# Performance work log

Measured on AMD Instinct MI355X. Metric: run time of the kernel, lower is better.

## Reference

```python
import jax, jax.numpy as jnp
import numpy as np

NUM_JOINTS = 140
NUM_VERTICES = 13059
NUM_BONES = 28
BATCH = 512


def euler_zyx_to_rot(e):
    """e: [..., 3] Euler angles in (z, y, x) order -> [..., 3, 3] with R = Rz @ Ry @ Rx."""
    z, y, x = e[..., 0], e[..., 1], e[..., 2]
    cx, sx = jnp.cos(x), jnp.sin(x)
    cy, sy = jnp.cos(y), jnp.sin(y)
    cz, sz = jnp.cos(z), jnp.sin(z)
    r00 = cz * cy
    r01 = cz * sy * sx - sz * cx
    r02 = cz * sy * cx + sz * sx
    r10 = sz * cy
    r11 = sz * sy * sx + cz * cx
    r12 = sz * sy * cx - cz * sx
    r20 = -sy
    r21 = cy * sx
    r22 = cy * cx
    R = jnp.stack([r00, r01, r02, r10, r11, r12, r20, r21, r22], axis=-1)
    return R.reshape(e.shape[:-1] + (3, 3))


def _mouse_forward(pose, bone_lengths, center_bone_length, trans, scale,
                   v_template, t_pose_joints, weights, parent, bone_mapper):
    B = pose.shape[0]
    Jn = NUM_JOINTS
    dt = pose.dtype

    bl = jax.nn.sigmoid(bone_lengths / 5.0) * 2.0            # [B, 28]
    R = euler_zyx_to_rot(pose.reshape(B, Jn, 3))             # [B, J, 3, 3]
    Jt = t_pose_joints                                       # [J, 3]

    # bone offsets for joints 1..J-1, scaled per bone_length_mapper
    off = Jt[1:] - Jt[parent[1:]]                            # [J-1, 3]
    blid = bone_mapper[1:]                                   # [J-1]
    bl_g = jnp.where(blid[None, :] >= 0,
                     jnp.take(bl, jnp.maximum(blid, 0), axis=1),
                     jnp.ones((), dt))                       # [B, J-1]
    # joint index 1 (position 0 in the [J-1] arrays) uses center_bone_length
    scale_per = bl_g.at[:, 0].set(center_bone_length[:, 0])
    off_b = off[None] * scale_per[..., None]                 # [B, J-1, 3]

    bottom = jnp.broadcast_to(jnp.array([0., 0., 0., 1.], dt), (B, Jn - 1, 1, 4))
    top = jnp.concatenate([R[:, 1:], off_b[..., None]], axis=-1)   # [B, J-1, 3, 4]
    A = jnp.concatenate([top, bottom], axis=-2)              # [B, J-1, 4, 4] local transforms

    root_t = jnp.broadcast_to(Jt[0], (B, 3))[..., None]      # [B, 3, 1]
    root_top = jnp.concatenate([R[:, 0], root_t], axis=-1)   # [B, 3, 4]
    root_bot = jnp.broadcast_to(jnp.array([0., 0., 0., 1.], dt), (B, 1, 4))
    G0 = jnp.concatenate([root_top, root_bot], axis=-2)      # [B, 4, 4]

    G_init = jnp.zeros((B, Jn, 4, 4), dt).at[:, 0].set(G0)

    def step(G, xs):
        i, p, Ai = xs                                        # Ai: [B, 4, 4]
        Gp = jnp.take(G, p, axis=1)                          # [B, 4, 4]
        Gi = Gp @ Ai
        return G.at[:, i].set(Gi), None

    idx = jnp.arange(1, Jn)
    G, _ = jax.lax.scan(step, G_init, (idx, parent[1:], jnp.swapaxes(A, 0, 1)))

    J_final = G[:, :, :3, 3]                                 # [B, J, 3]

    # subtract rest-pose joint contribution (relative transforms for LBS)
    Jh = jnp.concatenate([jnp.broadcast_to(Jt, (B, Jn, 3)),
                          jnp.zeros((B, Jn, 1), dt)], axis=-1)      # [B, J, 4]
    d = jnp.einsum('bjmn,bjn->bjm', G, Jh)                   # [B, J, 4]
    G_rel = jnp.concatenate([G[..., :3], (G[..., 3] - d)[..., None]], axis=-1)

    # linear blend skinning
    T = jnp.einsum('vj,bjmn->bvmn', weights, G_rel)          # [B, V, 4, 4]
    vh = jnp.concatenate([v_template, jnp.ones((NUM_VERTICES, 1), dt)], axis=-1)
    V = jnp.einsum('bvmn,vn->bvm', T[:, :, :3, :], vh)       # [B, V, 3]

    s = scale[:, 0][:, None, None]
    V = V * s + trans[:, None, :]
    J_out = J_final * s + trans[:, None, :]
    return V, J_out


def setup_inputs() -> dict:
    key = jax.random.key(0)
    ks = jax.random.split(key, 8)
    rng = np.random.default_rng(0)
    parent = np.zeros(NUM_JOINTS, dtype=np.int32)
    for i in range(1, NUM_JOINTS):
        parent[i] = rng.integers(0, i)                       # valid kinematic tree
    bone_mapper = rng.integers(-1, NUM_BONES, size=NUM_JOINTS).astype(np.int32)
    W = jax.random.uniform(ks[6], (NUM_VERTICES, NUM_JOINTS), jnp.float32)
    W = W / jnp.sum(W, axis=1, keepdims=True)                # row-stochastic skinning weights
    return {
        'pose': jax.random.normal(ks[0], (BATCH, NUM_JOINTS * 3), jnp.float32) * 0.2,
        'bone_lengths': jax.random.normal(ks[1], (BATCH, NUM_BONES), jnp.float32),
        'center_bone_length': jax.random.uniform(ks[2], (BATCH, 1), jnp.float32, 0.5, 1.5),
        'trans': jax.random.normal(ks[3], (BATCH, 3), jnp.float32),
        'scale': jax.random.uniform(ks[4], (BATCH, 1), jnp.float32, 0.5, 1.5),
        'v_template': jax.random.normal(ks[5], (NUM_VERTICES, 3), jnp.float32),
        't_pose_joints': jax.random.normal(ks[7], (NUM_JOINTS, 3), jnp.float32),
        'weights': W,
        'parent': jnp.asarray(parent),
        'bone_mapper': jnp.asarray(bone_mapper),
    }


def reference(pose, bone_lengths, center_bone_length, trans, scale,
              v_template, t_pose_joints, weights, parent, bone_mapper):
    return _mouse_forward(pose, bone_lengths, center_bone_length, trans, scale,
                          v_template, t_pose_joints, weights, parent, bone_mapper)
```

## Files before the change

kernel.cpp:

```cpp
#include <hip/hip_runtime.h>
#include <math.h>

#define NJ 140
#define NV 13059
#define NB 512
#define NBONES 28

#define MTILES 103
#define NBLK 12
#define KS 18
#define GRID_GEMM (MTILES*NBLK)

#define APREP_SLOTS (MTILES*KS*512)

typedef _Float16 f16x8 __attribute__((ext_vector_type(8)));
typedef float    f32x4 __attribute__((ext_vector_type(4)));

#define GL16(gp, lp) __builtin_amdgcn_global_load_lds( \
    (const __attribute__((address_space(1))) unsigned int*)(gp), \
    (__attribute__((address_space(3))) unsigned int*)(lp), 16, 0, 0)

__global__ __launch_bounds__(256) void prep_kernel(
    const float* __restrict__ pose,
    const float* __restrict__ bone_lengths,
    const float* __restrict__ cbl,
    const float* __restrict__ trans,
    const float* __restrict__ scale,
    const float* __restrict__ v_template,
    const float* __restrict__ t_pose,
    const int*   __restrict__ parent,
    const int*   __restrict__ bone_mapper,
    const float* __restrict__ weights,
    _Float16* __restrict__ Ap,
    _Float16* __restrict__ Bp,
    float* __restrict__ jout)
{
    const int t = threadIdx.x;

    if (blockIdx.x >= NB) {
        const int id  = blockIdx.x - NB;
        const int mt  = id / KS;
        const int ks  = id - mt*KS;
        const int row = t >> 1;
        const int q   = t & 1;
        const int v   = mt*128 + row;
        const int j0  = ks*8 + q*4;
        const int s   = (row >> 1) & 3;

        f16x8 oA, oB;
        #pragma unroll
        for (int i = 0; i < 8; ++i) { oA[i] = (_Float16)0.f; oB[i] = (_Float16)0.f; }

        if (v < NV && j0 + 3 < NJ) {
            float x = v_template[v*3+0];
            float y = v_template[v*3+1];
            float z = v_template[v*3+2];
            const float4 w4 = *(const float4*)(weights + (size_t)v*NJ + j0);
            oA[0] = (_Float16)(w4.x*x); oA[1] = (_Float16)(w4.x*y);
            oA[2] = (_Float16)(w4.x*z); oA[3] = (_Float16)w4.x;
            oA[4] = (_Float16)(w4.y*x); oA[5] = (_Float16)(w4.y*y);
            oA[6] = (_Float16)(w4.y*z); oA[7] = (_Float16)w4.y;
            oB[0] = (_Float16)(w4.z*x); oB[1] = (_Float16)(w4.z*y);
            oB[2] = (_Float16)(w4.z*z); oB[3] = (_Float16)w4.z;
            oB[4] = (_Float16)(w4.w*x); oB[5] = (_Float16)(w4.w*y);
            oB[6] = (_Float16)(w4.w*z); oB[7] = (_Float16)w4.w;
        }
        const int base = ((2*q) ^ s) & ~1;
        _Float16* dst = Ap + (((size_t)id)*512 + row*4 + base)*8;
        if (s & 1) {
            *(f16x8*)dst       = oB;
            *(f16x8*)(dst + 8) = oA;
        } else {
            *(f16x8*)dst       = oA;
            *(f16x8*)(dst + 8) = oB;
        }
        return;
    }

    __shared__ float M0[NJ][12];
    __shared__ float M1[NJ][12];
    __shared__ int   a0[NJ];
    __shared__ int   a1[NJ];

    const int b = blockIdx.x;

    if (t < NJ) {
        const int j = t;
        float z = pose[b*(NJ*3) + 3*j + 0];
        float y = pose[b*(NJ*3) + 3*j + 1];
        float x = pose[b*(NJ*3) + 3*j + 2];
        float cx = cosf(x), sx = sinf(x);
        float cy = cosf(y), sy = sinf(y);
        float cz = cosf(z), sz = sinf(z);
        float r00 = cz*cy;
        float r01 = cz*sy*sx - sz*cx;
        float r02 = cz*sy*cx + sz*sx;
        float r10 = sz*cy;
        float r11 = sz*sy*sx + cz*cx;
        float r12 = sz*sy*cx - cz*sx;
        float r20 = -sy;
        float r21 = cy*sx;
        float r22 = cy*cx;
        float t0, t1, t2;
        int p = parent[j];
        if (j == 0) {
            t0 = t_pose[0]; t1 = t_pose[1]; t2 = t_pose[2];
        } else {
            float ox = t_pose[3*j+0] - t_pose[3*p+0];
            float oy = t_pose[3*j+1] - t_pose[3*p+1];
            float oz = t_pose[3*j+2] - t_pose[3*p+2];
            float s;
            if (j == 1) {
                s = cbl[b];
            } else {
                int blid = bone_mapper[j];
                if (blid >= 0) {
                    float bv = bone_lengths[b*NBONES + blid];
                    s = 2.0f / (1.0f + expf(-bv*0.2f));
                } else {
                    s = 1.0f;
                }
            }
            t0 = ox*s; t1 = oy*s; t2 = oz*s;
        }
        M0[j][0]=r00; M0[j][1]=r01; M0[j][2]=r02;  M0[j][3]=t0;
        M0[j][4]=r10; M0[j][5]=r11; M0[j][6]=r12;  M0[j][7]=t1;
        M0[j][8]=r20; M0[j][9]=r21; M0[j][10]=r22; M0[j][11]=t2;
        a0[j] = (j == 0) ? -1 : p;
    }
    __syncthreads();

    float* src = &M0[0][0]; float* dst = &M1[0][0];
    int* as = a0; int* ad = a1;
    for (int r = 0; r < 8; ++r) {
        if (t < NJ) {
            int a = as[t];
            const float* Mi = src + t*12;
            float* Do = dst + t*12;
            if (a >= 0) {
                const float* Mp = src + a*12;
                #pragma unroll
                for (int m = 0; m < 3; ++m) {
                    float p0 = Mp[m*4+0], p1 = Mp[m*4+1], p2 = Mp[m*4+2], p3 = Mp[m*4+3];
                    Do[m*4+0] = p0*Mi[0] + p1*Mi[4] + p2*Mi[8];
                    Do[m*4+1] = p0*Mi[1] + p1*Mi[5] + p2*Mi[9];
                    Do[m*4+2] = p0*Mi[2] + p1*Mi[6] + p2*Mi[10];
                    Do[m*4+3] = p0*Mi[3] + p1*Mi[7] + p2*Mi[11] + p3;
                }
                ad[t] = as[a];
            } else {
                #pragma unroll
                for (int e = 0; e < 12; ++e) Do[e] = Mi[e];
                ad[t] = -1;
            }
        }
        __syncthreads();
        float* tf = src; src = dst; dst = tf;
        int* ti = as; as = ad; ad = ti;
    }

    float* grl = dst;
    if (t < NJ) {
        const int j = t;
        const float* G = src + j*12;
        float sb = scale[b];
        float tr0 = trans[b*3+0], tr1 = trans[b*3+1], tr2 = trans[b*3+2];
        float* jo = jout + ((size_t)b*NJ + j)*3;
        jo[0] = G[3]*sb  + tr0;
        jo[1] = G[7]*sb  + tr1;
        jo[2] = G[11]*sb + tr2;
        float jx = t_pose[3*j+0], jy = t_pose[3*j+1], jz = t_pose[3*j+2];
        #pragma unroll
        for (int c = 0; c < 3; ++c) {
            float g0 = G[c*4+0], g1 = G[c*4+1], g2 = G[c*4+2];
            float g3 = G[c*4+3] - (g0*jx + g1*jy + g2*jz);
            grl[j*12 + c*4 + 0] = g0;
            grl[j*12 + c*4 + 1] = g1;
            grl[j*12 + c*4 + 2] = g2;
            grl[j*12 + c*4 + 3] = g3;
        }
    }
    __syncthreads();

    if (t < 216) {
        int c  = t / 72;
        int rr = t - c*72;
        int ks = rr >> 2;
        int ci = rr & 3;
        int nrow = b*3 + c;
        int nbp = nrow >> 7;
        int rl = nrow & 127;
        int j0 = ks*8 + ci*2;
        f16x8 o;
        #pragma unroll
        for (int i = 0; i < 8; ++i) o[i] = (_Float16)0.f;
        if (j0 < NJ) {
            o[0] = (_Float16)grl[j0*12 + c*4 + 0];
            o[1] = (_Float16)grl[j0*12 + c*4 + 1];
            o[2] = (_Float16)grl[j0*12 + c*4 + 2];
            o[3] = (_Float16)grl[j0*12 + c*4 + 3];
        }
        if (j0 + 1 < NJ) {
            o[4] = (_Float16)grl[(j0+1)*12 + c*4 + 0];
            o[5] = (_Float16)grl[(j0+1)*12 + c*4 + 1];
            o[6] = (_Float16)grl[(j0+1)*12 + c*4 + 2];
            o[7] = (_Float16)grl[(j0+1)*12 + c*4 + 3];
        }
        int cs = ci ^ ((rl >> 1) & 3);
        *(f16x8*)(Bp + ((size_t)(nbp*KS + ks)*512 + rl*4 + cs)*8) = o;
    }
}

__global__ __launch_bounds__(512, 6) void gemm_kernel(
    const _Float16* __restrict__ Ap,
    const _Float16* __restrict__ Bp,
    const float* __restrict__ scale,
    const float* __restrict__ trans,
    float* __restrict__ vout)
{
    __shared__ __align__(16) char smem[40960];
    _Float16 (*sA)[4096] = (_Float16(*)[4096])smem;
    _Float16 (*sB)[4096] = (_Float16(*)[4096])(smem + 24576);

    const int t    = threadIdx.x;
    const int lane = t & 63;
    const int wid  = t >> 6;
    const int ln   = lane & 15;
    const int kq   = lane >> 4;
    const int wm   = wid & 1;
    const int wn   = wid >> 1;

    const int q8 = GRID_GEMM >> 3;
    const int r8 = GRID_GEMM & 7;
    const int xcd = blockIdx.x & 7;
    const int idx = blockIdx.x >> 3;
    const int wgid = (xcd < r8 ? xcd*(q8+1) : r8*(q8+1) + (xcd-r8)*q8) + idx;

    const int mt = wgid / NBLK;
    const int nb = wgid - mt*NBLK;

    const _Float16* Ag = Ap + (size_t)mt*(KS*4096);
    const _Float16* Bg = Bp + (size_t)nb*(KS*4096);

    const int csl = kq ^ ((ln >> 1) & 3);
    const int afo = (wm*64 + ln)*32 + csl*8;
    const int bfo = (wn*32 + ln)*32 + csl*8;

    f32x4 acc[4][2];
    #pragma unroll
    for (int mi = 0; mi < 4; ++mi)
        #pragma unroll
        for (int ni = 0; ni < 2; ++ni)
            acc[mi][ni] = (f32x4){0.f, 0.f, 0.f, 0.f};

    #define STAGE_A(buf, ksv) GL16(Ag + (ksv)*4096 + t*8, &sA[buf][wid*512])
    #define STAGE_B(buf, ksv) GL16(Bg + (ksv)*4096 + t*8, &sB[buf][wid*512])

    auto compute = [&](int ba, int bb) {
        f16x8 af[4], bf[2];
        #pragma unroll
        for (int mi = 0; mi < 4; ++mi)
            af[mi] = *(const f16x8*)&sA[ba][afo + mi*512];
        #pragma unroll
        for (int ni = 0; ni < 2; ++ni)
            bf[ni] = *(const f16x8*)&sB[bb][bfo + ni*512];
        __builtin_amdgcn_s_setprio(1);
        #pragma unroll
        for (int mi = 0; mi < 4; ++mi)
            #pragma unroll
            for (int ni = 0; ni < 2; ++ni)
                acc[mi][ni] = __builtin_amdgcn_mfma_f32_16x16x32_f16(
                    af[mi], bf[ni], acc[mi][ni], 0, 0, 0);
        __builtin_amdgcn_s_setprio(0);
    };

    #define STEP(j, bBn, bAn, bAc, bBc) do { \
        asm volatile("s_waitcnt vmcnt(1)" ::: "memory"); \
        __builtin_amdgcn_s_barrier(); \
        STAGE_B(bBn, (j) + 1); \
        STAGE_A(bAn, (j) + 2); \
        compute(bAc, bBc); } while (0)

    STAGE_B(0, 0);
    STAGE_A(0, 0);
    STAGE_A(1, 1);

    #pragma unroll 1
    for (int i = 0; i < 12; i += 6) {
        STEP(i + 0, 1, 2, 0, 0);
        STEP(i + 1, 0, 0, 1, 1);
        STEP(i + 2, 1, 1, 2, 0);
        STEP(i + 3, 0, 2, 0, 1);
        STEP(i + 4, 1, 0, 1, 0);
        STEP(i + 5, 0, 1, 2, 1);
    }
    STEP(12, 1, 2, 0, 0);
    STEP(13, 0, 0, 1, 1);
    STEP(14, 1, 1, 2, 0);
    STEP(15, 0, 2, 0, 1);
    asm volatile("s_waitcnt vmcnt(1)" ::: "memory");
    __builtin_amdgcn_s_barrier();
    STAGE_B(1, 17);
    compute(1, 0);
    asm volatile("s_waitcnt vmcnt(0)" ::: "memory");
    __builtin_amdgcn_s_barrier();
    compute(2, 1);

    #undef STEP
    #undef STAGE_A
    #undef STAGE_B

    float* Ct    = (float*)smem;
    float* es_l  = (float*)(smem + 33792);
    float* etr_l = (float*)(smem + 34304);

    const int vgA = t/3, crA = t - 3*vgA;

    #pragma unroll 1
    for (int h = 0; h < 2; ++h) {
        __syncthreads();
        if ((wn >> 1) == h) {
            #pragma unroll
            for (int mi = 0; mi < 4; ++mi)
                #pragma unroll
                for (int ni = 0; ni < 2; ++ni)
                    *(f32x4*)&Ct[((wn&1)*32 + ni*16 + ln)*132
                                 + wm*64 + mi*16 + kq*4] = acc[mi][ni];
        }
        if (h == 0 && t < 128) {
            int n = nb*128 + t;
            es_l[t]  = scale[n/3];
            etr_l[t] = trans[n];
        }
        __syncthreads();

        const int n0   = nb*128 + h*64;
        const int bq0  = n0/3;
        const int off0 = 3*bq0 - n0;
        const int bqN  = (n0 + 63)/3 - bq0 + 1;

        #pragma unroll 1
        for (int bqi = 0; bqi < bqN; ++bqi) {
            const long long base = (long long)(bq0 + bqi)*(NV*3)
                                 + (long long)mt*384;
            if (t < 384) {
                int nrel = off0 + 3*bqi + crA;
                if (nrel >= 0 && nrel < 64 && mt*128 + vgA < NV) {
                    int nf = h*64 + nrel;
                    vout[base + t] =
                        Ct[nrel*132 + vgA]*es_l[nf] + etr_l[nf];
                }
            }
        }
    }
}

extern "C" void kernel_launch(void* const* d_in, const int* in_sizes, int n_in,
                              void* d_out, int out_size, void* d_ws, size_t ws_size,
                              hipStream_t stream) {
    const float* pose         = (const float*)d_in[0];
    const float* bone_lengths = (const float*)d_in[1];
    const float* cbl          = (const float*)d_in[2];
    const float* trans        = (const float*)d_in[3];
    const float* scale        = (const float*)d_in[4];
    const float* v_template   = (const float*)d_in[5];
    const float* t_pose       = (const float*)d_in[6];
    const float* weights      = (const float*)d_in[7];
    const int*   parent       = (const int*)d_in[8];
    const int*   bone_mapper  = (const int*)d_in[9];

    float* vout = (float*)d_out;
    float* jout = vout + (size_t)NB*NV*3;

    _Float16* Ap = (_Float16*)d_ws;
    _Float16* Bp = Ap + (size_t)APREP_SLOTS*8;

    prep_kernel<<<NB + MTILES*KS, 256, 0, stream>>>(
        pose, bone_lengths, cbl, trans, scale, v_template, t_pose,
        parent, bone_mapper, weights, Ap, Bp, jout);

    gemm_kernel<<<GRID_GEMM, 512, 0, stream>>>(Ap, Bp, scale, trans, vout);
}
```

Before: 144.7 us.

## Fuse A-operand construction into GEMM and drop the pre-packed A buffer

```diff
diff --git a/kernel.cpp b/kernel.cpp
--- a/kernel.cpp
+++ b/kernel.cpp
@@ -11,8 +11,6 @@
 #define KS 18
 #define GRID_GEMM (MTILES*NBLK)
 
-#define APREP_SLOTS (MTILES*KS*512)
-
 typedef _Float16 f16x8 __attribute__((ext_vector_type(8)));
 typedef float    f32x4 __attribute__((ext_vector_type(4)));
 
@@ -20,62 +18,19 @@
     (const __attribute__((address_space(1))) unsigned int*)(gp), \
     (__attribute__((address_space(3))) unsigned int*)(lp), 16, 0, 0)
 
-__global__ __launch_bounds__(256) void prep_kernel(
+__global__ __launch_bounds__(256) void kin_kernel(
     const float* __restrict__ pose,
     const float* __restrict__ bone_lengths,
     const float* __restrict__ cbl,
     const float* __restrict__ trans,
     const float* __restrict__ scale,
-    const float* __restrict__ v_template,
     const float* __restrict__ t_pose,
     const int*   __restrict__ parent,
     const int*   __restrict__ bone_mapper,
-    const float* __restrict__ weights,
-    _Float16* __restrict__ Ap,
     _Float16* __restrict__ Bp,
     float* __restrict__ jout)
 {
     const int t = threadIdx.x;
-
-    if (blockIdx.x >= NB) {
-        const int id  = blockIdx.x - NB;
-        const int mt  = id / KS;
-        const int ks  = id - mt*KS;
-        const int row = t >> 1;
-        const int q   = t & 1;
-        const int v   = mt*128 + row;
-        const int j0  = ks*8 + q*4;
-        const int s   = (row >> 1) & 3;
-
-        f16x8 oA, oB;
-        #pragma unroll
-        for (int i = 0; i < 8; ++i) { oA[i] = (_Float16)0.f; oB[i] = (_Float16)0.f; }
-
-        if (v < NV && j0 + 3 < NJ) {
-            float x = v_template[v*3+0];
-            float y = v_template[v*3+1];
-            float z = v_template[v*3+2];
-            const float4 w4 = *(const float4*)(weights + (size_t)v*NJ + j0);
-            oA[0] = (_Float16)(w4.x*x); oA[1] = (_Float16)(w4.x*y);
-            oA[2] = (_Float16)(w4.x*z); oA[3] = (_Float16)w4.x;
-            oA[4] = (_Float16)(w4.y*x); oA[5] = (_Float16)(w4.y*y);
-            oA[6] = (_Float16)(w4.y*z); oA[7] = (_Float16)w4.y;
-            oB[0] = (_Float16)(w4.z*x); oB[1] = (_Float16)(w4.z*y);
-            oB[2] = (_Float16)(w4.z*z); oB[3] = (_Float16)w4.z;
-            oB[4] = (_Float16)(w4.w*x); oB[5] = (_Float16)(w4.w*y);
-            oB[6] = (_Float16)(w4.w*z); oB[7] = (_Float16)w4.w;
-        }
-        const int base = ((2*q) ^ s) & ~1;
-        _Float16* dst = Ap + (((size_t)id)*512 + row*4 + base)*8;
-        if (s & 1) {
-            *(f16x8*)dst       = oB;
-            *(f16x8*)(dst + 8) = oA;
-        } else {
-            *(f16x8*)dst       = oA;
-            *(f16x8*)(dst + 8) = oB;
-        }
-        return;
-    }
 
     __shared__ float M0[NJ][12];
     __shared__ float M1[NJ][12];
@@ -212,7 +167,8 @@
 }
 
 __global__ __launch_bounds__(512, 6) void gemm_kernel(
-    const _Float16* __restrict__ Ap,
+    const float* __restrict__ weights,
+    const float* __restrict__ v_template,
     const _Float16* __restrict__ Bp,
     const float* __restrict__ scale,
     const float* __restrict__ trans,
@@ -220,7 +176,7 @@
 {
     __shared__ __align__(16) char smem[40960];
     _Float16 (*sA)[4096] = (_Float16(*)[4096])smem;
-    _Float16 (*sB)[4096] = (_Float16(*)[4096])(smem + 24576);
+    _Float16 (*sB)[4096] = (_Float16(*)[4096])(smem + 16384);
 
     const int t    = threadIdx.x;
     const int lane = t & 63;
@@ -239,8 +195,18 @@
     const int mt = wgid / NBLK;
     const int nb = wgid - mt*NBLK;
 
-    const _Float16* Ag = Ap + (size_t)mt*(KS*4096);
     const _Float16* Bg = Bp + (size_t)nb*(KS*4096);
+
+    const int arow = t >> 2;
+    const int ajp  = t & 3;
+    const int v    = mt*128 + arow;
+    const int vc   = v < NV ? v : NV-1;
+    const float xg = v_template[vc*3+0];
+    const float yg = v_template[vc*3+1];
+    const float zg = v_template[vc*3+2];
+    const int wbase = vc*NJ + ajp*2;
+    const int wlim  = NV*NJ - 2;
+    const int awoff = (arow*4 + (ajp ^ ((arow >> 1) & 3)))*8;
 
     const int csl = kq ^ ((ln >> 1) & 3);
     const int afo = (wm*64 + ln)*32 + csl*8;
@@ -253,7 +219,16 @@
         for (int ni = 0; ni < 2; ++ni)
             acc[mi][ni] = (f32x4){0.f, 0.f, 0.f, 0.f};
 
-    #define STAGE_A(buf, ksv) GL16(Ag + (ksv)*4096 + t*8, &sA[buf][wid*512])
+    #define WLOAD(ksv) \
+        (*(const float2*)&weights[ (wbase + (ksv)*8 < wlim) ? \
+                                   (wbase + (ksv)*8) : wlim ])
+    #define AWRITE(buf, wv) do { \
+        f16x8 o_; \
+        o_[0]=(_Float16)((wv).x*xg); o_[1]=(_Float16)((wv).x*yg); \
+        o_[2]=(_Float16)((wv).x*zg); o_[3]=(_Float16)((wv).x); \
+        o_[4]=(_Float16)((wv).y*xg); o_[5]=(_Float16)((wv).y*yg); \
+        o_[6]=(_Float16)((wv).y*zg); o_[7]=(_Float16)((wv).y); \
+        *(f16x8*)&sA[buf][awoff] = o_; } while (0)
     #define STAGE_B(buf, ksv) GL16(Bg + (ksv)*4096 + t*8, &sB[buf][wid*512])
 
     auto compute = [&](int ba, int bb) {
@@ -274,41 +249,50 @@
         __builtin_amdgcn_s_setprio(0);
     };
 
-    #define STEP(j, bBn, bAn, bAc, bBc) do { \
+    float2 wvA, wvB;
+
+    #define STEP(j, aW, aR, bL, bR, WC, WN) do { \
         asm volatile("s_waitcnt vmcnt(1)" ::: "memory"); \
+        asm volatile("s_waitcnt lgkmcnt(0)" ::: "memory"); \
         __builtin_amdgcn_s_barrier(); \
-        STAGE_B(bBn, (j) + 1); \
-        STAGE_A(bAn, (j) + 2); \
-        compute(bAc, bBc); } while (0)
-
+        WN = WLOAD((j) + 2); \
+        AWRITE(aW, WC); \
+        STAGE_B(bL, (j) + 2); \
+        compute(aR, bR); } while (0)
+
+    wvA = WLOAD(0);
     STAGE_B(0, 0);
-    STAGE_A(0, 0);
-    STAGE_A(1, 1);
+    wvB = WLOAD(1);
+    STAGE_B(1, 1);
+    AWRITE(0, wvA);
 
     #pragma unroll 1
     for (int i = 0; i < 12; i += 6) {
-        STEP(i + 0, 1, 2, 0, 0);
-        STEP(i + 1, 0, 0, 1, 1);
-        STEP(i + 2, 1, 1, 2, 0);
-        STEP(i + 3, 0, 2, 0, 1);
-        STEP(i + 4, 1, 0, 1, 0);
-        STEP(i + 5, 0, 1, 2, 1);
-    }
-    STEP(12, 1, 2, 0, 0);
-    STEP(13, 0, 0, 1, 1);
-    STEP(14, 1, 1, 2, 0);
-    STEP(15, 0, 2, 0, 1);
+        STEP(i + 0, 1, 0, 2, 0, wvB, wvA);
+        STEP(i + 1, 0, 1, 0, 1, wvA, wvB);
+        STEP(i + 2, 1, 0, 1, 2, wvB, wvA);
+        STEP(i + 3, 0, 1, 2, 0, wvA, wvB);
+        STEP(i + 4, 1, 0, 0, 1, wvB, wvA);
+        STEP(i + 5, 0, 1, 1, 2, wvA, wvB);
+    }
+    STEP(12, 1, 0, 2, 0, wvB, wvA);
+    STEP(13, 0, 1, 0, 1, wvA, wvB);
+    STEP(14, 1, 0, 1, 2, wvB, wvA);
+    STEP(15, 0, 1, 2, 0, wvA, wvB);
     asm volatile("s_waitcnt vmcnt(1)" ::: "memory");
+    asm volatile("s_waitcnt lgkmcnt(0)" ::: "memory");
     __builtin_amdgcn_s_barrier();
-    STAGE_B(1, 17);
-    compute(1, 0);
+    AWRITE(1, wvB);
+    compute(0, 1);
     asm volatile("s_waitcnt vmcnt(0)" ::: "memory");
+    asm volatile("s_waitcnt lgkmcnt(0)" ::: "memory");
     __builtin_amdgcn_s_barrier();
-    compute(2, 1);
+    compute(1, 2);
 
     #undef STEP
-    #undef STAGE_A
     #undef STAGE_B
+    #undef AWRITE
+    #undef WLOAD
 
     float* Ct    = (float*)smem;
     float* es_l  = (float*)(smem + 33792);
@@ -372,12 +356,12 @@
     float* vout = (float*)d_out;
     float* jout = vout + (size_t)NB*NV*3;
 
-    _Float16* Ap = (_Float16*)d_ws;
-    _Float16* Bp = Ap + (size_t)APREP_SLOTS*8;
-
-    prep_kernel<<<NB + MTILES*KS, 256, 0, stream>>>(
-        pose, bone_lengths, cbl, trans, scale, v_template, t_pose,
-        parent, bone_mapper, weights, Ap, Bp, jout);
-
-    gemm_kernel<<<GRID_GEMM, 512, 0, stream>>>(Ap, Bp, scale, trans, vout);
+    _Float16* Bp = (_Float16*)d_ws;
+
+    kin_kernel<<<NB, 256, 0, stream>>>(
+        pose, bone_lengths, cbl, trans, scale, t_pose,
+        parent, bone_mapper, Bp, jout);
+
+    gemm_kernel<<<GRID_GEMM, 512, 0, stream>>>(
+        weights, v_template, Bp, scale, trans, vout);
 }
```

After: 167.0 us. 15.4% more time.
